# Kernel optimization log

Measured on AMD Instinct MI355X. Metric: run time of the kernel, lower is better.

Reference implementation:

```python
import jax, jax.numpy as jnp
import numpy as np

B = 65536       # batch size
C = 100         # num classes (len(cls_num_list))
ALPHA = 0.01    # soft-label blend weight
TAU = 2.0       # init arg tau
TEMP = 2.0      # distillation temperature
EPS = 1e-9


def _soft_ce(logits, soft_targets):
    # -(soft * log softmax(logits)).sum(1).mean()
    return -(soft_targets * jax.nn.log_softmax(logits, axis=1)).sum(axis=1).mean()


def _inverse_prior(prior):
    idx0 = jnp.argsort(prior)            # ascending sort permutation
    value = prior[idx0]                  # sorted values
    idx1 = jnp.argsort(idx0)             # rank of each element
    idx2 = prior.shape[0] - 1 - idx1     # mirrored rank
    return value[idx2]


def setup_inputs():
    key = jax.random.key(0)
    ks = jax.random.split(key, 8)
    cls_num = np.arange(500, 0, -5).astype(np.float32)  # matches init cls_num_list
    prior = jnp.asarray(cls_num / cls_num.sum(), dtype=jnp.float32)
    return {
        "output_logits": jax.random.normal(ks[0], (B, C), jnp.float32),
        "target": jax.random.randint(ks[1], (B,), 0, C),
        "cos_feature": jax.random.normal(ks[2], (C, C), jnp.float32),
        "old_pred": jax.random.normal(ks[3], (B, C), jnp.float32),
        "expert1_logits": jax.random.normal(ks[4], (B, C), jnp.float32),
        "expert2_logits": jax.random.normal(ks[5], (B, C), jnp.float32),
        "expert3_logits": jax.random.normal(ks[6], (B, C), jnp.float32),
        "output": jax.random.normal(ks[7], (B, C), jnp.float32),
        "prior": prior,
        "epoch": 5,
    }


def reference(output_logits, target, cos_feature, old_pred, expert1_logits,
              expert2_logits, expert3_logits, output, prior, epoch):
    num_classes = prior.shape[0]
    # ---- convert_to_soft_labels (vectorized: gather rows of sim matrix, softmax, blend) ----
    one_hot = jax.nn.one_hot(target, num_classes, dtype=jnp.float32)          # [B,C]
    sim_probs = jax.nn.softmax(cos_feature, axis=1)[target]                   # [B,C]
    label = (1.0 - ALPHA) * one_hot + ALPHA * sim_probs

    # ---- three expert soft cross-entropies ----
    log_prior = jnp.log(prior + EPS)
    loss = _soft_ce(expert1_logits, label)
    loss = loss + _soft_ce(expert2_logits + log_prior, label)
    inv_prior = _inverse_prior(prior)
    loss = loss + _soft_ce(expert3_logits + log_prior - TAU * jnp.log(inv_prior + EPS), label)

    # ---- bincount-normalized summed logits ----
    counts = jnp.bincount(target, length=num_classes).astype(jnp.float32)     # [C]
    num = counts[target][:, None]                                             # [B,1]
    expert_sum_logits = output / num                                          # [B,C]

    # ---- masked KL distillation (only rows where teacher argmax == target) ----
    teacher_index = jnp.argmax(old_pred, axis=1)                              # argmax(softmax)=argmax
    mask = (teacher_index == target).astype(jnp.float32)                      # [B]
    t = jax.nn.softmax(old_pred / TEMP, axis=1)                               # teacher probs
    s = jax.nn.log_softmax(expert_sum_logits / TEMP, axis=1)                  # student log-probs
    log_t = jnp.where(t > 0, jnp.log(t), 0.0)
    kl_per = (t * (log_t - s)).sum(axis=1)                                    # [B] per-row KL
    n_sel = mask.sum()
    kl_loss = jnp.where(n_sel > 0, (kl_per * mask).sum() / jnp.maximum(n_sel, 1.0), 0.0)
    kl_loss = kl_loss * (TEMP ** 2) * 3.0

    return loss, kl_loss, expert_sum_logits
```

## Files before the change

kernel.cpp:

```cpp
#include <hip/hip_runtime.h>
#include <math.h>

#define B_N 65536
#define C_N 100
constexpr float ALPHA = 0.01f;
constexpr float TAU   = 2.0f;
constexpr float TEMP  = 2.0f;
constexpr float EPSF  = 1e-9f;
constexpr float NEG_SENT = -1.0e30f;

template<int CTRL>
__device__ __forceinline__ float fadd_dpp(float x) {
    return x + __int_as_float(__builtin_amdgcn_update_dpp(
        0, __float_as_int(x), CTRL, 0xF, 0xF, true));
}
__device__ __forceinline__ float rowsum32(float x) {
    x = fadd_dpp<0xB1>(x);
    x = fadd_dpp<0x4E>(x);
    x = fadd_dpp<0x124>(x);
    x = fadd_dpp<0x128>(x);
    x = fadd_dpp<0x142>(x);
    return x;
}
template<int CTRL>
__device__ __forceinline__ void amax_dpp(unsigned &hi, unsigned &lo) {
    const unsigned yh = (unsigned)__builtin_amdgcn_update_dpp(0, (int)hi, CTRL, 0xF, 0xF, true);
    const unsigned yl = (unsigned)__builtin_amdgcn_update_dpp(0, (int)lo, CTRL, 0xF, 0xF, true);
    const bool take = (yh > hi) || (yh == hi && yl > lo);
    hi = take ? yh : hi;
    lo = take ? yl : lo;
}
__device__ __forceinline__ void rowamax32(unsigned &hi, unsigned &lo) {
    amax_dpp<0xB1>(hi, lo);
    amax_dpp<0x4E>(hi, lo);
    amax_dpp<0x124>(hi, lo);
    amax_dpp<0x128>(hi, lo);
    amax_dpp<0x142>(hi, lo);
}

__device__ __forceinline__ float wsum(float v) {
    #pragma unroll
    for (int o = 32; o; o >>= 1) v += __shfl_xor(v, o);
    return v;
}

__global__ void prep_k(const float* __restrict__ cosf, const float* __restrict__ prior,
                       const int* __restrict__ target,
                       float* __restrict__ sm, float* __restrict__ lp, float* __restrict__ c3,
                       int* __restrict__ counts) {
    const int b = blockIdx.x;
    if (b < 256) {
        __shared__ int h[C_N];
        for (int i = threadIdx.x; i < C_N; i += blockDim.x) h[i] = 0;
        __syncthreads();
        const int gid = b * blockDim.x + threadIdx.x;
        const int stride = 256 * blockDim.x;
        for (int i = gid; i < B_N; i += stride) atomicAdd(&h[target[i]], 1);
        __syncthreads();
        for (int i = threadIdx.x; i < C_N; i += blockDim.x)
            if (h[i]) atomicAdd(&counts[i], h[i]);
    } else if (b == 256) {
        __shared__ float sp[C_N];
        __shared__ float val[C_N];
        const int t = threadIdx.x;
        if (t < C_N) sp[t] = prior[t];
        __syncthreads();
        int rank = 0;
        float lpi = 0.f;
        if (t < C_N) {
            const float pi = sp[t];
            for (int j = 0; j < C_N; ++j) {
                const float pj = sp[j];
                rank += (pj < pi) || (pj == pi && j < t);
            }
            val[rank] = pi;
            lpi = __logf(pi + EPSF);
            lp[t] = lpi;
        }
        __syncthreads();
        if (t < C_N) {
            const float inv = val[C_N - 1 - rank];
            c3[t] = lpi - TAU * __logf(inv + EPSF);
        }
    } else {
        const int gw = (b - 257) * 4 + (threadIdx.x >> 6);
        const int lane = threadIdx.x & 63;
        for (int row = gw; row < C_N; row += 16) {
            const float* rp = cosf + row * C_N;
            const float v0 = rp[lane];
            const bool has1 = (lane + 64) < C_N;
            const float v1 = has1 ? rp[lane + 64] : -INFINITY;
            float m = fmaxf(v0, v1);
            #pragma unroll
            for (int o = 32; o; o >>= 1) m = fmaxf(m, __shfl_xor(m, o));
            const float e0 = __expf(v0 - m);
            const float e1 = has1 ? __expf(v1 - m) : 0.f;
            const float s = wsum(e0 + e1);
            const float is = 1.0f / s;
            sm[row * C_N + lane] = e0 * is;
            if (has1) sm[row * C_N + lane + 64] = e1 * is;
        }
    }
}

#define NBLK 8192

__launch_bounds__(256)
__global__ void main_k(const int* __restrict__ target,
                       const float* __restrict__ e1p, const float* __restrict__ e2p,
                       const float* __restrict__ e3p, const float* __restrict__ opp,
                       const float* __restrict__ outp,
                       const float* __restrict__ sm, const float* __restrict__ lp,
                       const float* __restrict__ c3, const int* __restrict__ counts,
                       float* __restrict__ dout,
                       float* __restrict__ ploss, float* __restrict__ pkl, float* __restrict__ pn) {
    const int lane = threadIdx.x & 63;
    const int gl   = lane & 31;
    const int half = lane >> 5;
    const int wslot = threadIdx.x >> 6;
    const int gw   = blockIdx.x * 4 + wslot;
    const bool act = gl < 25;
    const int c0 = 4 * gl;

    const int row = 2 * gw + half;
    const int tgt = target[row];
    const float rc = 1.0f / (float)counts[tgt];
    const int base = row * C_N;

    float4 LP = make_float4(0,0,0,0), CO = make_float4(0,0,0,0);
    float4 E1, E2, E3, OP, OU, SM;
    E1 = E2 = E3 = OP = OU = make_float4(NEG_SENT, NEG_SENT, NEG_SENT, NEG_SENT);
    SM = make_float4(0,0,0,0);
    if (act) {
        LP = *(const float4*)(lp + c0);
        CO = *(const float4*)(c3 + c0);
        E1 = *(const float4*)(e1p + base + c0);
        E2 = *(const float4*)(e2p + base + c0);
        E3 = *(const float4*)(e3p + base + c0);
        OP = *(const float4*)(opp + base + c0);
        OU = *(const float4*)(outp + base + c0);
        SM = *(const float4*)(sm + tgt * C_N + c0);
    }

    const float la0 = (1.0f - ALPHA) * (c0     == tgt) + ALPHA * SM.x;
    const float la1 = (1.0f - ALPHA) * (c0 + 1 == tgt) + ALPHA * SM.y;
    const float la2 = (1.0f - ALPHA) * (c0 + 2 == tgt) + ALPHA * SM.z;
    const float la3 = (1.0f - ALPHA) * (c0 + 3 == tgt) + ALPHA * SM.w;

    const float l20 = E2.x + LP.x, l21 = E2.y + LP.y, l22 = E2.z + LP.z, l23 = E2.w + LP.w;
    const float l30 = E3.x + CO.x, l31 = E3.y + CO.y, l32 = E3.z + CO.z, l33 = E3.w + CO.w;

    float s1 = __expf(E1.x) + __expf(E1.y) + __expf(E1.z) + __expf(E1.w);
    float s2 = __expf(l20) + __expf(l21) + __expf(l22) + __expf(l23);
    float s3 = __expf(l30) + __expf(l31) + __expf(l32) + __expf(l33);
    float dt = la0 * (E1.x + l20 + l30) + la1 * (E1.y + l21 + l31)
             + la2 * (E1.z + l22 + l32) + la3 * (E1.w + l23 + l33);

    const float a0 = OP.x * 0.5f, a1 = OP.y * 0.5f, a2 = OP.z * 0.5f, a3 = OP.w * 0.5f;
    const float p0 = __expf(a0), p1 = __expf(a1), p2 = __expf(a2), p3 = __expf(a3);
    float zt = p0 + p1 + p2 + p3;

    float bv = OP.x; int bi = c0;
    if (OP.y > bv) { bv = OP.y; bi = c0 + 1; }
    if (OP.z > bv) { bv = OP.z; bi = c0 + 2; }
    if (OP.w > bv) { bv = OP.w; bi = c0 + 3; }
    unsigned bb = __float_as_uint(bv);
    bb = ((int)bb < 0) ? ~bb : (bb | 0x80000000u);
    unsigned khi = bb, klo = (unsigned)~bi;

    const float es0 = OU.x * rc, es1 = OU.y * rc, es2 = OU.z * rc, es3 = OU.w * rc;
    const float x0 = es0 * 0.5f, x1 = es1 * 0.5f, x2 = es2 * 0.5f, x3 = es3 * 0.5f;
    float zs = __expf(x0) + __expf(x1) + __expf(x2) + __expf(x3);
    float D  = p0 * (a0 - x0) + p1 * (a1 - x1) + p2 * (a2 - x2) + p3 * (a3 - x3);

    s1 = rowsum32(s1);
    s2 = rowsum32(s2);
    s3 = rowsum32(s3);
    dt = rowsum32(dt);
    zt = rowsum32(zt);
    zs = rowsum32(zs);
    D  = rowsum32(D);
    rowamax32(khi, klo);

    const float ce  = __logf(s1 * s2 * s3) - dt;
    const int   mi  = (int)~klo;
    const float rzt = 1.0f / zt;
    const float kl  = D * rzt + __logf(zs * rzt);
    const bool  sel = (mi == tgt);

    if (act) {
        *(float2*)(dout + 2 + base + c0)     = make_float2(es0, es1);
        *(float2*)(dout + 2 + base + c0 + 2) = make_float2(es2, es3);
    }

    const float klm = sel ? kl : 0.f;
    const float nm  = sel ? 1.f : 0.f;
    const float lossW = __shfl(ce, 16) + __shfl(ce, 48);
    const float klW   = __shfl(klm, 16) + __shfl(klm, 48);
    const float nW    = __shfl(nm, 16) + __shfl(nm, 48);

    __shared__ float bl[4], bk[4], bn[4];
    if (lane == 0) { bl[wslot] = lossW; bk[wslot] = klW; bn[wslot] = nW; }
    __syncthreads();
    if (threadIdx.x == 0) {
        ploss[blockIdx.x] = bl[0] + bl[1] + bl[2] + bl[3];
        pkl[blockIdx.x]   = bk[0] + bk[1] + bk[2] + bk[3];
        pn[blockIdx.x]    = bn[0] + bn[1] + bn[2] + bn[3];
    }
}

__global__ void final_k(const float* __restrict__ ploss, const float* __restrict__ pkl,
                        const float* __restrict__ pn, float* __restrict__ dout) {
    __shared__ float sl[256], sk[256], sn[256];
    const int t = threadIdx.x;
    float l = 0.f, k = 0.f, n = 0.f;
    for (int i = t; i < NBLK; i += 256) { l += ploss[i]; k += pkl[i]; n += pn[i]; }
    sl[t] = l; sk[t] = k; sn[t] = n;
    __syncthreads();
    for (int s = 128; s; s >>= 1) {
        if (t < s) { sl[t] += sl[t + s]; sk[t] += sk[t + s]; sn[t] += sn[t + s]; }
        __syncthreads();
    }
    if (t == 0) {
        dout[0] = sl[0] / (float)B_N;
        const float kl = (sn[0] > 0.f) ? (sk[0] / fmaxf(sn[0], 1.f)) : 0.f;
        dout[1] = kl * (TEMP * TEMP) * 3.0f;
    }
}

extern "C" void kernel_launch(void* const* d_in, const int* in_sizes, int n_in,
                              void* d_out, int out_size, void* d_ws, size_t ws_size,
                              hipStream_t stream) {
    const int*   target = (const int*)  d_in[1];
    const float* cosf   = (const float*)d_in[2];
    const float* oldp   = (const float*)d_in[3];
    const float* e1     = (const float*)d_in[4];
    const float* e2     = (const float*)d_in[5];
    const float* e3     = (const float*)d_in[6];
    const float* outp   = (const float*)d_in[7];
    const float* prior  = (const float*)d_in[8];

    float* ws    = (float*)d_ws;
    float* sm    = ws;
    float* lp    = ws + 10000;
    float* c3    = ws + 10100;
    int*   cnts  = (int*)(ws + 10200);
    float* ploss = ws + 10304;
    float* pkl   = ploss + NBLK;
    float* pn    = pkl + NBLK;

    hipMemsetAsync(cnts, 0, C_N * sizeof(int), stream);
    prep_k<<<261, 256, 0, stream>>>(cosf, prior, target, sm, lp, c3, cnts);
    main_k<<<NBLK, 256, 0, stream>>>(target, e1, e2, e3, oldp, outp,
                                     sm, lp, c3, cnts, (float*)d_out, ploss, pkl, pn);
    final_k<<<1, 256, 0, stream>>>(ploss, pkl, pn, (float*)d_out);
}
```

Baseline: 53.16 us.

## Process multiple row pairs per wave in larger blocks with shared-memory constants

Grid shrinks from 8192 blocks of 256 threads to 512 blocks of 1024 threads. Each wave loops over four row pairs, accumulating loss and KL locally, and defers its output stores until after the block reduction. Per-class reciprocals of counts, log-prior and combined prior terms are staged in shared memory, which removes repeated global loads and fewer block partials feed the final reduction. The cost is a serial loop with unroll 1 that may expose load latency, plus extra registers for the deferred stores, which could reduce memory-level parallelism in this bandwidth-bound kernel.

Result: slower. 142.6 us (+168.2%).

```diff
diff --git a/kernel.cpp b/kernel.cpp
--- a/kernel.cpp
+++ b/kernel.cpp
@@ -103,9 +103,11 @@
     }
 }
 
-#define NBLK 8192
-
-__launch_bounds__(256)
+#define NBLK 512
+#define WPB 16
+#define PAIRS 4
+
+__launch_bounds__(1024, 8)
 __global__ void main_k(const int* __restrict__ target,
                        const float* __restrict__ e1p, const float* __restrict__ e2p,
                        const float* __restrict__ e3p, const float* __restrict__ opp,
@@ -114,98 +116,137 @@
                        const float* __restrict__ c3, const int* __restrict__ counts,
                        float* __restrict__ dout,
                        float* __restrict__ ploss, float* __restrict__ pkl, float* __restrict__ pn) {
-    const int lane = threadIdx.x & 63;
+    const int t    = threadIdx.x;
+    const int lane = t & 63;
     const int gl   = lane & 31;
     const int half = lane >> 5;
-    const int wslot = threadIdx.x >> 6;
-    const int gw   = blockIdx.x * 4 + wslot;
+    const int wslot = t >> 6;
     const bool act = gl < 25;
     const int c0 = 4 * gl;
 
-    const int row = 2 * gw + half;
-    const int tgt = target[row];
-    const float rc = 1.0f / (float)counts[tgt];
-    const int base = row * C_N;
+    __shared__ __align__(16) float s_rcp[104];
+    __shared__ __align__(16) float s_lp[104];
+    __shared__ __align__(16) float s_c3[104];
+    __shared__ float bl[WPB], bk[WPB], bn[WPB];
+
+    if (t < C_N) {
+        s_rcp[t] = 1.0f / (float)counts[t];
+        s_lp[t]  = lp[t];
+        s_c3[t]  = c3[t];
+    }
+    __syncthreads();
 
     float4 LP = make_float4(0,0,0,0), CO = make_float4(0,0,0,0);
-    float4 E1, E2, E3, OP, OU, SM;
-    E1 = E2 = E3 = OP = OU = make_float4(NEG_SENT, NEG_SENT, NEG_SENT, NEG_SENT);
-    SM = make_float4(0,0,0,0);
     if (act) {
-        LP = *(const float4*)(lp + c0);
-        CO = *(const float4*)(c3 + c0);
-        E1 = *(const float4*)(e1p + base + c0);
-        E2 = *(const float4*)(e2p + base + c0);
-        E3 = *(const float4*)(e3p + base + c0);
-        OP = *(const float4*)(opp + base + c0);
-        OU = *(const float4*)(outp + base + c0);
-        SM = *(const float4*)(sm + tgt * C_N + c0);
-    }
-
-    const float la0 = (1.0f - ALPHA) * (c0     == tgt) + ALPHA * SM.x;
-    const float la1 = (1.0f - ALPHA) * (c0 + 1 == tgt) + ALPHA * SM.y;
-    const float la2 = (1.0f - ALPHA) * (c0 + 2 == tgt) + ALPHA * SM.z;
-    const float la3 = (1.0f - ALPHA) * (c0 + 3 == tgt) + ALPHA * SM.w;
-
-    const float l20 = E2.x + LP.x, l21 = E2.y + LP.y, l22 = E2.z + LP.z, l23 = E2.w + LP.w;
-    const float l30 = E3.x + CO.x, l31 = E3.y + CO.y, l32 = E3.z + CO.z, l33 = E3.w + CO.w;
-
-    float s1 = __expf(E1.x) + __expf(E1.y) + __expf(E1.z) + __expf(E1.w);
-    float s2 = __expf(l20) + __expf(l21) + __expf(l22) + __expf(l23);
-    float s3 = __expf(l30) + __expf(l31) + __expf(l32) + __expf(l33);
-    float dt = la0 * (E1.x + l20 + l30) + la1 * (E1.y + l21 + l31)
-             + la2 * (E1.z + l22 + l32) + la3 * (E1.w + l23 + l33);
-
-    const float a0 = OP.x * 0.5f, a1 = OP.y * 0.5f, a2 = OP.z * 0.5f, a3 = OP.w * 0.5f;
-    const float p0 = __expf(a0), p1 = __expf(a1), p2 = __expf(a2), p3 = __expf(a3);
-    float zt = p0 + p1 + p2 + p3;
-
-    float bv = OP.x; int bi = c0;
-    if (OP.y > bv) { bv = OP.y; bi = c0 + 1; }
-    if (OP.z > bv) { bv = OP.z; bi = c0 + 2; }
-    if (OP.w > bv) { bv = OP.w; bi = c0 + 3; }
-    unsigned bb = __float_as_uint(bv);
-    bb = ((int)bb < 0) ? ~bb : (bb | 0x80000000u);
-    unsigned khi = bb, klo = (unsigned)~bi;
-
-    const float es0 = OU.x * rc, es1 = OU.y * rc, es2 = OU.z * rc, es3 = OU.w * rc;
-    const float x0 = es0 * 0.5f, x1 = es1 * 0.5f, x2 = es2 * 0.5f, x3 = es3 * 0.5f;
-    float zs = __expf(x0) + __expf(x1) + __expf(x2) + __expf(x3);
-    float D  = p0 * (a0 - x0) + p1 * (a1 - x1) + p2 * (a2 - x2) + p3 * (a3 - x3);
-
-    s1 = rowsum32(s1);
-    s2 = rowsum32(s2);
-    s3 = rowsum32(s3);
-    dt = rowsum32(dt);
-    zt = rowsum32(zt);
-    zs = rowsum32(zs);
-    D  = rowsum32(D);
-    rowamax32(khi, klo);
-
-    const float ce  = __logf(s1 * s2 * s3) - dt;
-    const int   mi  = (int)~klo;
-    const float rzt = 1.0f / zt;
-    const float kl  = D * rzt + __logf(zs * rzt);
-    const bool  sel = (mi == tgt);
-
-    if (act) {
-        *(float2*)(dout + 2 + base + c0)     = make_float2(es0, es1);
-        *(float2*)(dout + 2 + base + c0 + 2) = make_float2(es2, es3);
-    }
-
-    const float klm = sel ? kl : 0.f;
-    const float nm  = sel ? 1.f : 0.f;
-    const float lossW = __shfl(ce, 16) + __shfl(ce, 48);
-    const float klW   = __shfl(klm, 16) + __shfl(klm, 48);
-    const float nW    = __shfl(nm, 16) + __shfl(nm, 48);
-
-    __shared__ float bl[4], bk[4], bn[4];
+        LP = *(const float4*)(s_lp + c0);
+        CO = *(const float4*)(s_c3 + c0);
+    }
+
+    const int pair0 = blockIdx.x * (WPB * PAIRS) + wslot * PAIRS;
+
+    int tg[PAIRS];
+    #pragma unroll
+    for (int q = 0; q < PAIRS; ++q) tg[q] = target[2 * (pair0 + q) + half];
+    float rcq[PAIRS];
+    #pragma unroll
+    for (int q = 0; q < PAIRS; ++q) rcq[q] = s_rcp[tg[q]];
+
+    float lossA = 0.f, klA = 0.f, nA = 0.f;
+    float esv[PAIRS][4];
+
+    #pragma unroll 1
+    for (int q = 0; q < PAIRS; ++q) {
+        const int row = 2 * (pair0 + q) + half;
+        const int tgt = tg[q];
+        const float rc = rcq[q];
+        const int base = row * C_N;
+
+        float4 E1, E2, E3, OP, OU, SM;
+        E1 = E2 = E3 = OP = OU = make_float4(NEG_SENT, NEG_SENT, NEG_SENT, NEG_SENT);
+        SM = make_float4(0,0,0,0);
+        if (act) {
+            E1 = *(const float4*)(e1p + base + c0);
+            E2 = *(const float4*)(e2p + base + c0);
+            E3 = *(const float4*)(e3p + base + c0);
+            OP = *(const float4*)(opp + base + c0);
+            OU = *(const float4*)(outp + base + c0);
+            SM = *(const float4*)(sm + tgt * C_N + c0);
+        }
+
+        const float la0 = (1.0f - ALPHA) * (c0     == tgt) + ALPHA * SM.x;
+        const float la1 = (1.0f - ALPHA) * (c0 + 1 == tgt) + ALPHA * SM.y;
+        const float la2 = (1.0f - ALPHA) * (c0 + 2 == tgt) + ALPHA * SM.z;
+        const float la3 = (1.0f - ALPHA) * (c0 + 3 == tgt) + ALPHA * SM.w;
+
+        const float l20 = E2.x + LP.x, l21 = E2.y + LP.y, l22 = E2.z + LP.z, l23 = E2.w + LP.w;
+        const float l30 = E3.x + CO.x, l31 = E3.y + CO.y, l32 = E3.z + CO.z, l33 = E3.w + CO.w;
+
+        float s1 = __expf(E1.x) + __expf(E1.y) + __expf(E1.z) + __expf(E1.w);
+        float s2 = __expf(l20) + __expf(l21) + __expf(l22) + __expf(l23);
+        float s3 = __expf(l30) + __expf(l31) + __expf(l32) + __expf(l33);
+        float dt = la0 * (E1.x + l20 + l30) + la1 * (E1.y + l21 + l31)
+                 + la2 * (E1.z + l22 + l32) + la3 * (E1.w + l23 + l33);
+
+        const float a0 = OP.x * 0.5f, a1 = OP.y * 0.5f, a2 = OP.z * 0.5f, a3 = OP.w * 0.5f;
+        const float p0 = __expf(a0), p1 = __expf(a1), p2 = __expf(a2), p3 = __expf(a3);
+        float zt = p0 + p1 + p2 + p3;
+
+        float bv = OP.x; int bi = c0;
+        if (OP.y > bv) { bv = OP.y; bi = c0 + 1; }
+        if (OP.z > bv) { bv = OP.z; bi = c0 + 2; }
+        if (OP.w > bv) { bv = OP.w; bi = c0 + 3; }
+        unsigned bb = __float_as_uint(bv);
+        bb = ((int)bb < 0) ? ~bb : (bb | 0x80000000u);
+        unsigned khi = bb, klo = (unsigned)~bi;
+
+        const float es0 = OU.x * rc, es1 = OU.y * rc, es2 = OU.z * rc, es3 = OU.w * rc;
+        const float x0 = es0 * 0.5f, x1 = es1 * 0.5f, x2 = es2 * 0.5f, x3 = es3 * 0.5f;
+        float zs = __expf(x0) + __expf(x1) + __expf(x2) + __expf(x3);
+        float D  = p0 * (a0 - x0) + p1 * (a1 - x1) + p2 * (a2 - x2) + p3 * (a3 - x3);
+
+        s1 = rowsum32(s1);
+        s2 = rowsum32(s2);
+        s3 = rowsum32(s3);
+        dt = rowsum32(dt);
+        zt = rowsum32(zt);
+        zs = rowsum32(zs);
+        D  = rowsum32(D);
+        rowamax32(khi, klo);
+
+        const float ce  = __logf(s1 * s2 * s3) - dt;
+        const int   mi  = (int)~klo;
+        const float rzt = 1.0f / zt;
+        const float kl  = D * rzt + __logf(zs * rzt);
+        const bool  own = (gl == 16);
+        const bool  sel = own && (mi == tgt);
+
+        lossA += own ? ce : 0.f;
+        klA   += sel ? kl : 0.f;
+        nA    += sel ? 1.f : 0.f;
+
+        esv[q][0] = es0; esv[q][1] = es1; esv[q][2] = es2; esv[q][3] = es3;
+    }
+
+    const float lossW = __shfl(lossA, 16) + __shfl(lossA, 48);
+    const float klW   = __shfl(klA, 16) + __shfl(klA, 48);
+    const float nW    = __shfl(nA, 16) + __shfl(nA, 48);
+
     if (lane == 0) { bl[wslot] = lossW; bk[wslot] = klW; bn[wslot] = nW; }
     __syncthreads();
-    if (threadIdx.x == 0) {
-        ploss[blockIdx.x] = bl[0] + bl[1] + bl[2] + bl[3];
-        pkl[blockIdx.x]   = bk[0] + bk[1] + bk[2] + bk[3];
-        pn[blockIdx.x]    = bn[0] + bn[1] + bn[2] + bn[3];
+    if (t == 0) {
+        float L = 0.f, K = 0.f, N = 0.f;
+        #pragma unroll
+        for (int i = 0; i < WPB; ++i) { L += bl[i]; K += bk[i]; N += bn[i]; }
+        ploss[blockIdx.x] = L; pkl[blockIdx.x] = K; pn[blockIdx.x] = N;
+    }
+
+    if (act) {
+        #pragma unroll
+        for (int q = 0; q < PAIRS; ++q) {
+            const int base = (2 * (pair0 + q) + half) * C_N;
+            *(float2*)(dout + 2 + base + c0)     = make_float2(esv[q][0], esv[q][1]);
+            *(float2*)(dout + 2 + base + c0 + 2) = make_float2(esv[q][2], esv[q][3]);
+        }
     }
 }
 
@@ -251,7 +292,7 @@
 
     hipMemsetAsync(cnts, 0, C_N * sizeof(int), stream);
     prep_k<<<261, 256, 0, stream>>>(cosf, prior, target, sm, lp, c3, cnts);
-    main_k<<<NBLK, 256, 0, stream>>>(target, e1, e2, e3, oldp, outp,
-                                     sm, lp, c3, cnts, (float*)d_out, ploss, pkl, pn);
+    main_k<<<NBLK, 1024, 0, stream>>>(target, e1, e2, e3, oldp, outp,
+                                      sm, lp, c3, cnts, (float*)d_out, ploss, pkl, pn);
     final_k<<<1, 256, 0, stream>>>(ploss, pkl, pn, (float*)d_out);
 }
```

## Stage row tiles through LDS with persistent chunked blocks and prefolded prior weights

Applied to the files above, without the earlier changes.

The main kernel now launches 1024 blocks of 512 threads, and each block walks 4 chunks of 16 rows. Each chunk's five input tiles are loaded into shared memory with fully coalesced float4 copies and then read per row from LDS. The prior terms are prefolded in the prep kernel into multiplicative weights (p+eps, exp(c3)) and a combined additive term, which removes per-element adds before the exponentials. This adds two block barriers per chunk and 32KB of LDS per block, which may limit occupancy. Only 400 of 512 threads take part in the loads, and loads are not overlapped with compute.

New measurement: 67.99 us. 27.9% more time.

```diff
diff --git a/kernel.cpp b/kernel.cpp
--- a/kernel.cpp
+++ b/kernel.cpp
@@ -46,7 +46,8 @@
 
 __global__ void prep_k(const float* __restrict__ cosf, const float* __restrict__ prior,
                        const int* __restrict__ target,
-                       float* __restrict__ sm, float* __restrict__ lp, float* __restrict__ c3,
+                       float* __restrict__ sm, float* __restrict__ w2,
+                       float* __restrict__ w3, float* __restrict__ Ht,
                        int* __restrict__ counts) {
     const int b = blockIdx.x;
     if (b < 256) {
@@ -66,21 +67,23 @@
         if (t < C_N) sp[t] = prior[t];
         __syncthreads();
         int rank = 0;
-        float lpi = 0.f;
+        float lpi = 0.f, pi = 0.f;
         if (t < C_N) {
-            const float pi = sp[t];
+            pi = sp[t];
             for (int j = 0; j < C_N; ++j) {
                 const float pj = sp[j];
                 rank += (pj < pi) || (pj == pi && j < t);
             }
             val[rank] = pi;
             lpi = __logf(pi + EPSF);
-            lp[t] = lpi;
         }
         __syncthreads();
         if (t < C_N) {
             const float inv = val[C_N - 1 - rank];
-            c3[t] = lpi - TAU * __logf(inv + EPSF);
+            const float c3v = lpi - TAU * __logf(inv + EPSF);
+            w2[t] = pi + EPSF;
+            w3[t] = __expf(c3v);
+            Ht[t] = lpi + c3v;
         }
     } else {
         const int gw = (b - 257) * 4 + (threadIdx.x >> 6);
@@ -103,109 +106,151 @@
     }
 }
 
-#define NBLK 8192
-
-__launch_bounds__(256)
+#define NBLK 1024
+#define TPB 512
+#define RPC 16
+#define CHUNKS 4
+#define CHF (RPC * C_N)
+
+__launch_bounds__(TPB, 8)
 __global__ void main_k(const int* __restrict__ target,
                        const float* __restrict__ e1p, const float* __restrict__ e2p,
                        const float* __restrict__ e3p, const float* __restrict__ opp,
                        const float* __restrict__ outp,
-                       const float* __restrict__ sm, const float* __restrict__ lp,
-                       const float* __restrict__ c3, const int* __restrict__ counts,
+                       const float* __restrict__ sm, const float* __restrict__ w2p,
+                       const float* __restrict__ w3p, const float* __restrict__ Hp,
+                       const int* __restrict__ counts,
                        float* __restrict__ dout,
                        float* __restrict__ ploss, float* __restrict__ pkl, float* __restrict__ pn) {
-    const int lane = threadIdx.x & 63;
+    __shared__ __align__(16) float lsE1[CHF];
+    __shared__ __align__(16) float lsE2[CHF];
+    __shared__ __align__(16) float lsE3[CHF];
+    __shared__ __align__(16) float lsOP[CHF];
+    __shared__ __align__(16) float lsOU[CHF];
+    __shared__ float bl[8], bk[8], bn[8];
+
+    const int t    = threadIdx.x;
+    const int lane = t & 63;
     const int gl   = lane & 31;
     const int half = lane >> 5;
-    const int wslot = threadIdx.x >> 6;
-    const int gw   = blockIdx.x * 4 + wslot;
+    const int w    = t >> 6;
     const bool act = gl < 25;
     const int c0 = 4 * gl;
-
-    const int row = 2 * gw + half;
-    const int tgt = target[row];
-    const float rc = 1.0f / (float)counts[tgt];
-    const int base = row * C_N;
-
-    float4 LP = make_float4(0,0,0,0), CO = make_float4(0,0,0,0);
-    float4 E1, E2, E3, OP, OU, SM;
-    E1 = E2 = E3 = OP = OU = make_float4(NEG_SENT, NEG_SENT, NEG_SENT, NEG_SENT);
-    SM = make_float4(0,0,0,0);
+    const bool own = (gl == 16);
+    const int lr = 2 * w + half;
+
+    float4 W2 = make_float4(0,0,0,0), W3 = make_float4(0,0,0,0), HH = make_float4(0,0,0,0);
     if (act) {
-        LP = *(const float4*)(lp + c0);
-        CO = *(const float4*)(c3 + c0);
-        E1 = *(const float4*)(e1p + base + c0);
-        E2 = *(const float4*)(e2p + base + c0);
-        E3 = *(const float4*)(e3p + base + c0);
-        OP = *(const float4*)(opp + base + c0);
-        OU = *(const float4*)(outp + base + c0);
-        SM = *(const float4*)(sm + tgt * C_N + c0);
-    }
-
-    const float la0 = (1.0f - ALPHA) * (c0     == tgt) + ALPHA * SM.x;
-    const float la1 = (1.0f - ALPHA) * (c0 + 1 == tgt) + ALPHA * SM.y;
-    const float la2 = (1.0f - ALPHA) * (c0 + 2 == tgt) + ALPHA * SM.z;
-    const float la3 = (1.0f - ALPHA) * (c0 + 3 == tgt) + ALPHA * SM.w;
-
-    const float l20 = E2.x + LP.x, l21 = E2.y + LP.y, l22 = E2.z + LP.z, l23 = E2.w + LP.w;
-    const float l30 = E3.x + CO.x, l31 = E3.y + CO.y, l32 = E3.z + CO.z, l33 = E3.w + CO.w;
-
-    float s1 = __expf(E1.x) + __expf(E1.y) + __expf(E1.z) + __expf(E1.w);
-    float s2 = __expf(l20) + __expf(l21) + __expf(l22) + __expf(l23);
-    float s3 = __expf(l30) + __expf(l31) + __expf(l32) + __expf(l33);
-    float dt = la0 * (E1.x + l20 + l30) + la1 * (E1.y + l21 + l31)
-             + la2 * (E1.z + l22 + l32) + la3 * (E1.w + l23 + l33);
-
-    const float a0 = OP.x * 0.5f, a1 = OP.y * 0.5f, a2 = OP.z * 0.5f, a3 = OP.w * 0.5f;
-    const float p0 = __expf(a0), p1 = __expf(a1), p2 = __expf(a2), p3 = __expf(a3);
-    float zt = p0 + p1 + p2 + p3;
-
-    float bv = OP.x; int bi = c0;
-    if (OP.y > bv) { bv = OP.y; bi = c0 + 1; }
-    if (OP.z > bv) { bv = OP.z; bi = c0 + 2; }
-    if (OP.w > bv) { bv = OP.w; bi = c0 + 3; }
-    unsigned bb = __float_as_uint(bv);
-    bb = ((int)bb < 0) ? ~bb : (bb | 0x80000000u);
-    unsigned khi = bb, klo = (unsigned)~bi;
-
-    const float es0 = OU.x * rc, es1 = OU.y * rc, es2 = OU.z * rc, es3 = OU.w * rc;
-    const float x0 = es0 * 0.5f, x1 = es1 * 0.5f, x2 = es2 * 0.5f, x3 = es3 * 0.5f;
-    float zs = __expf(x0) + __expf(x1) + __expf(x2) + __expf(x3);
-    float D  = p0 * (a0 - x0) + p1 * (a1 - x1) + p2 * (a2 - x2) + p3 * (a3 - x3);
-
-    s1 = rowsum32(s1);
-    s2 = rowsum32(s2);
-    s3 = rowsum32(s3);
-    dt = rowsum32(dt);
-    zt = rowsum32(zt);
-    zs = rowsum32(zs);
-    D  = rowsum32(D);
-    rowamax32(khi, klo);
-
-    const float ce  = __logf(s1 * s2 * s3) - dt;
-    const int   mi  = (int)~klo;
-    const float rzt = 1.0f / zt;
-    const float kl  = D * rzt + __logf(zs * rzt);
-    const bool  sel = (mi == tgt);
-
-    if (act) {
-        *(float2*)(dout + 2 + base + c0)     = make_float2(es0, es1);
-        *(float2*)(dout + 2 + base + c0 + 2) = make_float2(es2, es3);
-    }
-
-    const float klm = sel ? kl : 0.f;
-    const float nm  = sel ? 1.f : 0.f;
-    const float lossW = __shfl(ce, 16) + __shfl(ce, 48);
-    const float klW   = __shfl(klm, 16) + __shfl(klm, 48);
-    const float nW    = __shfl(nm, 16) + __shfl(nm, 48);
-
-    __shared__ float bl[4], bk[4], bn[4];
-    if (lane == 0) { bl[wslot] = lossW; bk[wslot] = klW; bn[wslot] = nW; }
+        W2 = *(const float4*)(w2p + c0);
+        W3 = *(const float4*)(w3p + c0);
+        HH = *(const float4*)(Hp + c0);
+    }
+
+    float lossA = 0.f, klA = 0.f, nA = 0.f;
+
+    for (int c = 0; c < CHUNKS; ++c) {
+        const int row0 = blockIdx.x * (RPC * CHUNKS) + c * RPC;
+        const long fbase = (long)row0 * C_N;
+
+        __syncthreads();
+        if (t < CHF / 4) {
+            const float4 v1 = ((const float4*)(e1p + fbase))[t];
+            const float4 v2 = ((const float4*)(e2p + fbase))[t];
+            const float4 v3 = ((const float4*)(e3p + fbase))[t];
+            const float4 v4 = ((const float4*)(opp + fbase))[t];
+            const float4 v5 = ((const float4*)(outp + fbase))[t];
+            ((float4*)lsE1)[t] = v1;
+            ((float4*)lsE2)[t] = v2;
+            ((float4*)lsE3)[t] = v3;
+            ((float4*)lsOP)[t] = v4;
+            ((float4*)lsOU)[t] = v5;
+        }
+        __syncthreads();
+
+        const int row = row0 + lr;
+        const int tgt = target[row];
+        const float rc = 1.0f / (float)counts[tgt];
+        const int base = row * C_N;
+        const int lbase = lr * C_N;
+
+        float4 E1, E2, E3, OP, OU, SM;
+        E1 = E2 = E3 = OP = OU = make_float4(NEG_SENT, NEG_SENT, NEG_SENT, NEG_SENT);
+        SM = make_float4(0,0,0,0);
+        if (act) {
+            E1 = *(const float4*)(lsE1 + lbase + c0);
+            E2 = *(const float4*)(lsE2 + lbase + c0);
+            E3 = *(const float4*)(lsE3 + lbase + c0);
+            OP = *(const float4*)(lsOP + lbase + c0);
+            OU = *(const float4*)(lsOU + lbase + c0);
+            SM = *(const float4*)(sm + tgt * C_N + c0);
+        }
+
+        const float la0 = (1.0f - ALPHA) * (c0     == tgt) + ALPHA * SM.x;
+        const float la1 = (1.0f - ALPHA) * (c0 + 1 == tgt) + ALPHA * SM.y;
+        const float la2 = (1.0f - ALPHA) * (c0 + 2 == tgt) + ALPHA * SM.z;
+        const float la3 = (1.0f - ALPHA) * (c0 + 3 == tgt) + ALPHA * SM.w;
+        float s1 = __expf(E1.x) + __expf(E1.y) + __expf(E1.z) + __expf(E1.w);
+        float s2 = W2.x * __expf(E2.x) + W2.y * __expf(E2.y)
+                 + W2.z * __expf(E2.z) + W2.w * __expf(E2.w);
+        float s3 = W3.x * __expf(E3.x) + W3.y * __expf(E3.y)
+                 + W3.z * __expf(E3.z) + W3.w * __expf(E3.w);
+        float dt = la0 * (E1.x + E2.x + E3.x + HH.x)
+                 + la1 * (E1.y + E2.y + E3.y + HH.y)
+                 + la2 * (E1.z + E2.z + E3.z + HH.z)
+                 + la3 * (E1.w + E2.w + E3.w + HH.w);
+
+        const float a0 = OP.x * 0.5f, a1 = OP.y * 0.5f, a2 = OP.z * 0.5f, a3 = OP.w * 0.5f;
+        const float p0 = __expf(a0), p1 = __expf(a1), p2 = __expf(a2), p3 = __expf(a3);
+        float zt = p0 + p1 + p2 + p3;
+        float bv = OP.x; int bi = c0;
+        if (OP.y > bv) { bv = OP.y; bi = c0 + 1; }
+        if (OP.z > bv) { bv = OP.z; bi = c0 + 2; }
+        if (OP.w > bv) { bv = OP.w; bi = c0 + 3; }
+        unsigned bb = __float_as_uint(bv);
+        bb = ((int)bb < 0) ? ~bb : (bb | 0x80000000u);
+        unsigned khi = bb, klo = (unsigned)~bi;
+
+        const float es0 = OU.x * rc, es1 = OU.y * rc, es2 = OU.z * rc, es3 = OU.w * rc;
+        const float x0 = es0 * 0.5f, x1 = es1 * 0.5f, x2 = es2 * 0.5f, x3 = es3 * 0.5f;
+        float zs = __expf(x0) + __expf(x1) + __expf(x2) + __expf(x3);
+        float D  = p0 * (a0 - x0) + p1 * (a1 - x1) + p2 * (a2 - x2) + p3 * (a3 - x3);
+
+        if (act) {
+            *(float2*)(dout + 2 + base + c0)     = make_float2(es0, es1);
+            *(float2*)(dout + 2 + base + c0 + 2) = make_float2(es2, es3);
+        }
+
+        s1 = rowsum32(s1);
+        s2 = rowsum32(s2);
+        s3 = rowsum32(s3);
+        dt = rowsum32(dt);
+        zt = rowsum32(zt);
+        zs = rowsum32(zs);
+        D  = rowsum32(D);
+        rowamax32(khi, klo);
+
+        const float ce  = __logf(s1 * s2 * s3) - dt;
+        const int   mi  = (int)~klo;
+        const float rzt = 1.0f / zt;
+        const float kl  = D * rzt + __logf(zs * rzt);
+        const bool  sel = own && (mi == tgt);
+
+        lossA += own ? ce : 0.f;
+        klA   += sel ? kl : 0.f;
+        nA    += sel ? 1.f : 0.f;
+    }
+
+    const float lossW = __shfl(lossA, 16) + __shfl(lossA, 48);
+    const float klW   = __shfl(klA, 16) + __shfl(klA, 48);
+    const float nW    = __shfl(nA, 16) + __shfl(nA, 48);
+
+    if (lane == 0) { bl[w] = lossW; bk[w] = klW; bn[w] = nW; }
     __syncthreads();
-    if (threadIdx.x == 0) {
-        ploss[blockIdx.x] = bl[0] + bl[1] + bl[2] + bl[3];
-        pkl[blockIdx.x]   = bk[0] + bk[1] + bk[2] + bk[3];
-        pn[blockIdx.x]    = bn[0] + bn[1] + bn[2] + bn[3];
+    if (t == 0) {
+        float L = 0.f, K = 0.f, N = 0.f;
+        #pragma unroll
+        for (int i = 0; i < 8; ++i) { L += bl[i]; K += bk[i]; N += bn[i]; }
+        ploss[blockIdx.x] = L; pkl[blockIdx.x] = K; pn[blockIdx.x] = N;
     }
 }
 
@@ -242,16 +287,17 @@
 
     float* ws    = (float*)d_ws;
     float* sm    = ws;
-    float* lp    = ws + 10000;
-    float* c3    = ws + 10100;
-    int*   cnts  = (int*)(ws + 10200);
-    float* ploss = ws + 10304;
+    float* w2    = ws + 10016;
+    float* w3    = ws + 10120;
+    float* Ht    = ws + 10224;
+    int*   cnts  = (int*)(ws + 10328);
+    float* ploss = ws + 10432;
     float* pkl   = ploss + NBLK;
     float* pn    = pkl + NBLK;
 
     hipMemsetAsync(cnts, 0, C_N * sizeof(int), stream);
-    prep_k<<<261, 256, 0, stream>>>(cosf, prior, target, sm, lp, c3, cnts);
-    main_k<<<NBLK, 256, 0, stream>>>(target, e1, e2, e3, oldp, outp,
-                                     sm, lp, c3, cnts, (float*)d_out, ploss, pkl, pn);
+    prep_k<<<261, 256, 0, stream>>>(cosf, prior, target, sm, w2, w3, Ht, cnts);
+    main_k<<<NBLK, TPB, 0, stream>>>(target, e1, e2, e3, oldp, outp,
+                                     sm, w2, w3, Ht, cnts, (float*)d_out, ploss, pkl, pn);
     final_k<<<1, 256, 0, stream>>>(ploss, pkl, pn, (float*)d_out);
 }
```

## Split main kernel into element-parallel CE and teacher-student kernels with atomic row sums

Applied to the files above, without the earlier changes.

Replaces the row-per-half-wave fused kernel with two flat element-per-thread kernels: one computes the three expert CE partial sums, the other the distillation terms and argmax key. Per-row sums are built with wave-wide DPP reductions, with at most two rows per wave, and global atomics into per-row workspace arrays. A separate row finalize kernel and a smaller final reduction follow. Precomputed per-class multipliers turn the prior offsets into multiplies after exp. The aim is fully coalesced scalar access with no idle lanes, at the cost of many atomics, an extra 2.3MB memset and per-row arrays, and more launches.

Result: slower. 103.7 us (+95.0%).

```diff
diff --git a/kernel.cpp b/kernel.cpp
--- a/kernel.cpp
+++ b/kernel.cpp
@@ -3,50 +3,47 @@
 
 #define B_N 65536
 #define C_N 100
+#define NELEM (B_N * C_N)
 constexpr float ALPHA = 0.01f;
 constexpr float TAU   = 2.0f;
 constexpr float TEMP  = 2.0f;
 constexpr float EPSF  = 1e-9f;
-constexpr float NEG_SENT = -1.0e30f;
 
 template<int CTRL>
 __device__ __forceinline__ float fadd_dpp(float x) {
     return x + __int_as_float(__builtin_amdgcn_update_dpp(
         0, __float_as_int(x), CTRL, 0xF, 0xF, true));
 }
-__device__ __forceinline__ float rowsum32(float x) {
+__device__ __forceinline__ float dppsum64(float x) {
     x = fadd_dpp<0xB1>(x);
     x = fadd_dpp<0x4E>(x);
     x = fadd_dpp<0x124>(x);
     x = fadd_dpp<0x128>(x);
     x = fadd_dpp<0x142>(x);
+    x = fadd_dpp<0x143>(x);
     return x;
 }
-template<int CTRL>
-__device__ __forceinline__ void amax_dpp(unsigned &hi, unsigned &lo) {
-    const unsigned yh = (unsigned)__builtin_amdgcn_update_dpp(0, (int)hi, CTRL, 0xF, 0xF, true);
-    const unsigned yl = (unsigned)__builtin_amdgcn_update_dpp(0, (int)lo, CTRL, 0xF, 0xF, true);
-    const bool take = (yh > hi) || (yh == hi && yl > lo);
-    hi = take ? yh : hi;
-    lo = take ? yl : lo;
-}
-__device__ __forceinline__ void rowamax32(unsigned &hi, unsigned &lo) {
-    amax_dpp<0xB1>(hi, lo);
-    amax_dpp<0x4E>(hi, lo);
-    amax_dpp<0x124>(hi, lo);
-    amax_dpp<0x128>(hi, lo);
-    amax_dpp<0x142>(hi, lo);
-}
-
+__device__ __forceinline__ unsigned long long wmax64(unsigned long long k) {
+    #pragma unroll
+    for (int o = 32; o; o >>= 1) {
+        const unsigned long long t = __shfl_xor(k, o);
+        k = (t > k) ? t : k;
+    }
+    return k;
+}
 __device__ __forceinline__ float wsum(float v) {
     #pragma unroll
     for (int o = 32; o; o >>= 1) v += __shfl_xor(v, o);
     return v;
 }
+__device__ __forceinline__ unsigned div100(unsigned n) {
+    return __umulhi(n, 0x51EB851Fu) >> 5;
+}
 
 __global__ void prep_k(const float* __restrict__ cosf, const float* __restrict__ prior,
                        const int* __restrict__ target,
-                       float* __restrict__ sm, float* __restrict__ lp, float* __restrict__ c3,
+                       float* __restrict__ sm, float* __restrict__ w2,
+                       float* __restrict__ w3, float* __restrict__ Ht,
                        int* __restrict__ counts) {
     const int b = blockIdx.x;
     if (b < 256) {
@@ -66,21 +63,23 @@
         if (t < C_N) sp[t] = prior[t];
         __syncthreads();
         int rank = 0;
-        float lpi = 0.f;
+        float lpi = 0.f, pi = 0.f;
         if (t < C_N) {
-            const float pi = sp[t];
+            pi = sp[t];
             for (int j = 0; j < C_N; ++j) {
                 const float pj = sp[j];
                 rank += (pj < pi) || (pj == pi && j < t);
             }
             val[rank] = pi;
             lpi = __logf(pi + EPSF);
-            lp[t] = lpi;
         }
         __syncthreads();
         if (t < C_N) {
             const float inv = val[C_N - 1 - rank];
-            c3[t] = lpi - TAU * __logf(inv + EPSF);
+            const float c3v = lpi - TAU * __logf(inv + EPSF);
+            w2[t] = pi + EPSF;
+            w3[t] = __expf(c3v);
+            Ht[t] = lpi + c3v;
         }
     } else {
         const int gw = (b - 257) * 4 + (threadIdx.x >> 6);
@@ -103,119 +102,148 @@
     }
 }
 
-#define NBLK 8192
-
-__launch_bounds__(256)
-__global__ void main_k(const int* __restrict__ target,
-                       const float* __restrict__ e1p, const float* __restrict__ e2p,
-                       const float* __restrict__ e3p, const float* __restrict__ opp,
-                       const float* __restrict__ outp,
-                       const float* __restrict__ sm, const float* __restrict__ lp,
-                       const float* __restrict__ c3, const int* __restrict__ counts,
-                       float* __restrict__ dout,
-                       float* __restrict__ ploss, float* __restrict__ pkl, float* __restrict__ pn) {
+#define CTPB 256
+#define CBLK (NELEM / CTPB)
+
+__launch_bounds__(CTPB)
+__global__ void ce_k(const float* __restrict__ e1p, const float* __restrict__ e2p,
+                     const float* __restrict__ e3p, const int* __restrict__ target,
+                     const float* __restrict__ sm, const float* __restrict__ w2p,
+                     const float* __restrict__ w3p, const float* __restrict__ Hp,
+                     float* __restrict__ S1, float* __restrict__ S2,
+                     float* __restrict__ S3, float* __restrict__ DT) {
+    const int i = blockIdx.x * CTPB + threadIdx.x;
     const int lane = threadIdx.x & 63;
-    const int gl   = lane & 31;
-    const int half = lane >> 5;
-    const int wslot = threadIdx.x >> 6;
-    const int gw   = blockIdx.x * 4 + wslot;
-    const bool act = gl < 25;
-    const int c0 = 4 * gl;
-
-    const int row = 2 * gw + half;
+    const unsigned r = div100((unsigned)i);
+    const int col = i - (int)r * C_N;
+
+    const float v1 = e1p[i];
+    const float v2 = e2p[i];
+    const float v3 = e3p[i];
+    const int tgt = target[r];
+    const float smv = sm[tgt * C_N + col];
+    const float h   = Hp[col];
+    const float w2v = w2p[col];
+    const float w3v = w3p[col];
+
+    const float lab = ALPHA * smv + ((col == tgt) ? (1.0f - ALPHA) : 0.0f);
+    const float q1 = __expf(v1);
+    const float q2 = w2v * __expf(v2);
+    const float q3 = w3v * __expf(v3);
+    const float qd = lab * (v1 + v2 + v3 + h);
+
+    const unsigned rlo = (unsigned)__shfl((int)r, 0);
+    const unsigned rhi = (unsigned)__shfl((int)r, 63);
+    const bool isA = (r == rlo);
+
+    const float a1 = dppsum64(isA ? q1 : 0.f), b1 = dppsum64(isA ? 0.f : q1);
+    const float a2 = dppsum64(isA ? q2 : 0.f), b2 = dppsum64(isA ? 0.f : q2);
+    const float a3 = dppsum64(isA ? q3 : 0.f), b3 = dppsum64(isA ? 0.f : q3);
+    const float ad = dppsum64(isA ? qd : 0.f), bd = dppsum64(isA ? 0.f : qd);
+
+    if (lane == 63) {
+        atomicAdd(&S1[rlo], a1);
+        atomicAdd(&S2[rlo], a2);
+        atomicAdd(&S3[rlo], a3);
+        atomicAdd(&DT[rlo], ad);
+        if (rhi != rlo) {
+            atomicAdd(&S1[rhi], b1);
+            atomicAdd(&S2[rhi], b2);
+            atomicAdd(&S3[rhi], b3);
+            atomicAdd(&DT[rhi], bd);
+        }
+    }
+}
+
+__launch_bounds__(CTPB)
+__global__ void ts_k(const int* __restrict__ target,
+                     const float* __restrict__ opp, const float* __restrict__ oup,
+                     const int* __restrict__ cnts, float* __restrict__ dout,
+                     float* __restrict__ ZT, float* __restrict__ ZS,
+                     float* __restrict__ DD, unsigned long long* __restrict__ KEY) {
+    const int i = blockIdx.x * CTPB + threadIdx.x;
+    const int lane = threadIdx.x & 63;
+    const unsigned r = div100((unsigned)i);
+    const int col = i - (int)r * C_N;
+
+    const float op = opp[i];
+    const float ou = oup[i];
+    const int tgt = target[r];
+    const float rc = 1.0f / (float)cnts[tgt];
+    const float es = ou * rc;
+    dout[2 + i] = es;
+
+    const float a = 0.5f * op;
+    const float x = 0.5f * es;
+    const float p = __expf(a);
+    const float q = __expf(x);
+    const float d = p * (a - x);
+
+    unsigned bb = __float_as_uint(op);
+    bb = ((int)bb < 0) ? ~bb : (bb | 0x80000000u);
+    const unsigned long long key =
+        ((unsigned long long)bb << 32) | (unsigned)(~col);
+
+    const unsigned rlo = (unsigned)__shfl((int)r, 0);
+    const unsigned rhi = (unsigned)__shfl((int)r, 63);
+    const bool isA = (r == rlo);
+
+    const float azt = dppsum64(isA ? p : 0.f), bzt = dppsum64(isA ? 0.f : p);
+    const float azs = dppsum64(isA ? q : 0.f), bzs = dppsum64(isA ? 0.f : q);
+    const float add = dppsum64(isA ? d : 0.f), bdd = dppsum64(isA ? 0.f : d);
+    const unsigned long long kA = wmax64(isA ? key : 0ull);
+    const unsigned long long kB = wmax64(isA ? 0ull : key);
+
+    if (lane == 63) {
+        atomicAdd(&ZT[rlo], azt);
+        atomicAdd(&ZS[rlo], azs);
+        atomicAdd(&DD[rlo], add);
+        atomicMax(&KEY[rlo], kA);
+        if (rhi != rlo) {
+            atomicAdd(&ZT[rhi], bzt);
+            atomicAdd(&ZS[rhi], bzs);
+            atomicAdd(&DD[rhi], bdd);
+            atomicMax(&KEY[rhi], kB);
+        }
+    }
+}
+
+__global__ void rf_k(const int* __restrict__ target,
+                     const float* __restrict__ S1, const float* __restrict__ S2,
+                     const float* __restrict__ S3, const float* __restrict__ DT,
+                     const float* __restrict__ ZT, const float* __restrict__ ZS,
+                     const float* __restrict__ DD, const unsigned long long* __restrict__ KEY,
+                     float* __restrict__ pl, float* __restrict__ pk, float* __restrict__ pn) {
+    const int t = threadIdx.x;
+    const int row = blockIdx.x * 256 + t;
+    const float s1 = S1[row], s2 = S2[row], s3 = S3[row], dt = DT[row];
+    const float zt = ZT[row], zs = ZS[row], dd = DD[row];
+    const unsigned long long key = KEY[row];
+    const int mi = (int)(~(unsigned)key);
     const int tgt = target[row];
-    const float rc = 1.0f / (float)counts[tgt];
-    const int base = row * C_N;
-
-    float4 LP = make_float4(0,0,0,0), CO = make_float4(0,0,0,0);
-    float4 E1, E2, E3, OP, OU, SM;
-    E1 = E2 = E3 = OP = OU = make_float4(NEG_SENT, NEG_SENT, NEG_SENT, NEG_SENT);
-    SM = make_float4(0,0,0,0);
-    if (act) {
-        LP = *(const float4*)(lp + c0);
-        CO = *(const float4*)(c3 + c0);
-        E1 = *(const float4*)(e1p + base + c0);
-        E2 = *(const float4*)(e2p + base + c0);
-        E3 = *(const float4*)(e3p + base + c0);
-        OP = *(const float4*)(opp + base + c0);
-        OU = *(const float4*)(outp + base + c0);
-        SM = *(const float4*)(sm + tgt * C_N + c0);
-    }
-
-    const float la0 = (1.0f - ALPHA) * (c0     == tgt) + ALPHA * SM.x;
-    const float la1 = (1.0f - ALPHA) * (c0 + 1 == tgt) + ALPHA * SM.y;
-    const float la2 = (1.0f - ALPHA) * (c0 + 2 == tgt) + ALPHA * SM.z;
-    const float la3 = (1.0f - ALPHA) * (c0 + 3 == tgt) + ALPHA * SM.w;
-
-    const float l20 = E2.x + LP.x, l21 = E2.y + LP.y, l22 = E2.z + LP.z, l23 = E2.w + LP.w;
-    const float l30 = E3.x + CO.x, l31 = E3.y + CO.y, l32 = E3.z + CO.z, l33 = E3.w + CO.w;
-
-    float s1 = __expf(E1.x) + __expf(E1.y) + __expf(E1.z) + __expf(E1.w);
-    float s2 = __expf(l20) + __expf(l21) + __expf(l22) + __expf(l23);
-    float s3 = __expf(l30) + __expf(l31) + __expf(l32) + __expf(l33);
-    float dt = la0 * (E1.x + l20 + l30) + la1 * (E1.y + l21 + l31)
-             + la2 * (E1.z + l22 + l32) + la3 * (E1.w + l23 + l33);
-
-    const float a0 = OP.x * 0.5f, a1 = OP.y * 0.5f, a2 = OP.z * 0.5f, a3 = OP.w * 0.5f;
-    const float p0 = __expf(a0), p1 = __expf(a1), p2 = __expf(a2), p3 = __expf(a3);
-    float zt = p0 + p1 + p2 + p3;
-
-    float bv = OP.x; int bi = c0;
-    if (OP.y > bv) { bv = OP.y; bi = c0 + 1; }
-    if (OP.z > bv) { bv = OP.z; bi = c0 + 2; }
-    if (OP.w > bv) { bv = OP.w; bi = c0 + 3; }
-    unsigned bb = __float_as_uint(bv);
-    bb = ((int)bb < 0) ? ~bb : (bb | 0x80000000u);
-    unsigned khi = bb, klo = (unsigned)~bi;
-
-    const float es0 = OU.x * rc, es1 = OU.y * rc, es2 = OU.z * rc, es3 = OU.w * rc;
-    const float x0 = es0 * 0.5f, x1 = es1 * 0.5f, x2 = es2 * 0.5f, x3 = es3 * 0.5f;
-    float zs = __expf(x0) + __expf(x1) + __expf(x2) + __expf(x3);
-    float D  = p0 * (a0 - x0) + p1 * (a1 - x1) + p2 * (a2 - x2) + p3 * (a3 - x3);
-
-    s1 = rowsum32(s1);
-    s2 = rowsum32(s2);
-    s3 = rowsum32(s3);
-    dt = rowsum32(dt);
-    zt = rowsum32(zt);
-    zs = rowsum32(zs);
-    D  = rowsum32(D);
-    rowamax32(khi, klo);
 
     const float ce  = __logf(s1 * s2 * s3) - dt;
-    const int   mi  = (int)~klo;
     const float rzt = 1.0f / zt;
-    const float kl  = D * rzt + __logf(zs * rzt);
+    const float kl  = dd * rzt + __logf(zs * rzt);
     const bool  sel = (mi == tgt);
 
-    if (act) {
-        *(float2*)(dout + 2 + base + c0)     = make_float2(es0, es1);
-        *(float2*)(dout + 2 + base + c0 + 2) = make_float2(es2, es3);
-    }
-
-    const float klm = sel ? kl : 0.f;
-    const float nm  = sel ? 1.f : 0.f;
-    const float lossW = __shfl(ce, 16) + __shfl(ce, 48);
-    const float klW   = __shfl(klm, 16) + __shfl(klm, 48);
-    const float nW    = __shfl(nm, 16) + __shfl(nm, 48);
-
-    __shared__ float bl[4], bk[4], bn[4];
-    if (lane == 0) { bl[wslot] = lossW; bk[wslot] = klW; bn[wslot] = nW; }
+    __shared__ float sl[256], sk[256], sn[256];
+    sl[t] = ce;
+    sk[t] = sel ? kl : 0.f;
+    sn[t] = sel ? 1.f : 0.f;
     __syncthreads();
-    if (threadIdx.x == 0) {
-        ploss[blockIdx.x] = bl[0] + bl[1] + bl[2] + bl[3];
-        pkl[blockIdx.x]   = bk[0] + bk[1] + bk[2] + bk[3];
-        pn[blockIdx.x]    = bn[0] + bn[1] + bn[2] + bn[3];
-    }
-}
-
-__global__ void final_k(const float* __restrict__ ploss, const float* __restrict__ pkl,
-                        const float* __restrict__ pn, float* __restrict__ dout) {
+    for (int s = 128; s; s >>= 1) {
+        if (t < s) { sl[t] += sl[t + s]; sk[t] += sk[t + s]; sn[t] += sn[t + s]; }
+        __syncthreads();
+    }
+    if (t == 0) { pl[blockIdx.x] = sl[0]; pk[blockIdx.x] = sk[0]; pn[blockIdx.x] = sn[0]; }
+}
+
+__global__ void f2_k(const float* __restrict__ pl, const float* __restrict__ pk,
+                     const float* __restrict__ pn, float* __restrict__ dout) {
     __shared__ float sl[256], sk[256], sn[256];
     const int t = threadIdx.x;
-    float l = 0.f, k = 0.f, n = 0.f;
-    for (int i = t; i < NBLK; i += 256) { l += ploss[i]; k += pkl[i]; n += pn[i]; }
-    sl[t] = l; sk[t] = k; sn[t] = n;
+    sl[t] = pl[t]; sk[t] = pk[t]; sn[t] = pn[t];
     __syncthreads();
     for (int s = 128; s; s >>= 1) {
         if (t < s) { sl[t] += sl[t + s]; sk[t] += sk[t + s]; sn[t] += sn[t + s]; }
@@ -240,18 +268,31 @@
     const float* outp   = (const float*)d_in[7];
     const float* prior  = (const float*)d_in[8];
 
-    float* ws    = (float*)d_ws;
-    float* sm    = ws;
-    float* lp    = ws + 10000;
-    float* c3    = ws + 10100;
-    int*   cnts  = (int*)(ws + 10200);
-    float* ploss = ws + 10304;
-    float* pkl   = ploss + NBLK;
-    float* pn    = pkl + NBLK;
-
-    hipMemsetAsync(cnts, 0, C_N * sizeof(int), stream);
-    prep_k<<<261, 256, 0, stream>>>(cosf, prior, target, sm, lp, c3, cnts);
-    main_k<<<NBLK, 256, 0, stream>>>(target, e1, e2, e3, oldp, outp,
-                                     sm, lp, c3, cnts, (float*)d_out, ploss, pkl, pn);
-    final_k<<<1, 256, 0, stream>>>(ploss, pkl, pn, (float*)d_out);
-}
+    float* ws = (float*)d_ws;
+    float* S1 = ws;
+    float* S2 = S1 + B_N;
+    float* S3 = S2 + B_N;
+    float* DT = S3 + B_N;
+    float* ZT = DT + B_N;
+    float* ZS = ZT + B_N;
+    float* DD = ZS + B_N;
+    unsigned long long* KEY = (unsigned long long*)(DD + B_N);
+    float* after = (float*)(KEY + B_N);
+    float* sm   = after;
+    float* w2   = sm + 10000;
+    float* w3   = w2 + 104;
+    float* Ht   = w3 + 104;
+    int*   cnts = (int*)(Ht + 104);
+    float* pl   = (float*)(cnts + 104);
+    float* pk   = pl + 256;
+    float* pn   = pk + 256;
+
+    hipMemsetAsync(S1, 0, (size_t)9 * B_N * sizeof(float), stream);
+    hipMemsetAsync(cnts, 0, 104 * sizeof(int), stream);
+
+    prep_k<<<261, 256, 0, stream>>>(cosf, prior, target, sm, w2, w3, Ht, cnts);
+    ce_k<<<CBLK, CTPB, 0, stream>>>(e1, e2, e3, target, sm, w2, w3, Ht, S1, S2, S3, DT);
+    ts_k<<<CBLK, CTPB, 0, stream>>>(target, oldp, outp, cnts, (float*)d_out, ZT, ZS, DD, KEY);
+    rf_k<<<B_N / 256, 256, 0, stream>>>(target, S1, S2, S3, DT, ZT, ZS, DD, KEY, pl, pk, pn);
+    f2_k<<<1, 256, 0, stream>>>(pl, pk, pn, (float*)d_out);
+}
```
